# Optimization experiments

Hardware: AMD Instinct MI355X
Metric: run time of the kernel (lower is better)

The kernel has to match this reference:

```python
import jax, jax.numpy as jnp
import numpy as np

V, D, DU, H = 50000, 256, 1024, 128
TEMP = 0.01

def time_cosine_emb(t, d_model):
    half = d_model // 2
    div_term = jnp.exp(jnp.arange(half, dtype=jnp.float32) * (-np.log(10000.0) / half))
    scaled = t[..., None] * div_term  # (B, L, half)
    return jnp.concatenate([jnp.sin(scaled), jnp.cos(scaled)], axis=-1)

def setup_inputs() -> dict:
    key = jax.random.key(0)
    ks = jax.random.split(key, 12)
    B, L = 64, 2048
    q_seq = jax.random.randint(ks[0], (B, L), 0, V)
    r_seq = jax.random.randint(ks[1], (B, L), 0, 3)
    t_seq = jax.random.uniform(ks[2], (B, L), dtype=jnp.float32) * 1000.0
    mask = jnp.ones((B, L), dtype=jnp.float32)
    q_tab = jax.random.normal(ks[3], (V, D), dtype=jnp.float32) * 0.02
    q_tab = q_tab.at[0].set(0.0)  # padding_idx=0
    r_tab = jax.random.normal(ks[4], (3, D), dtype=jnp.float32) * 0.02
    r_tab = r_tab.at[0].set(0.0)  # padding_idx=0
    virtual_node = jax.random.normal(ks[5], (1, D), dtype=jnp.float32)
    Ws1 = jax.random.normal(ks[6], (H, 2 * D), dtype=jnp.float32) * (1.0 / np.sqrt(2 * D))
    bs1 = jnp.zeros((H,), dtype=jnp.float32)
    Ws2 = jax.random.normal(ks[7], (1, H), dtype=jnp.float32) * (1.0 / np.sqrt(H))
    bs2 = jnp.zeros((1,), dtype=jnp.float32)
    Wa = jax.random.normal(ks[8], (DU, D), dtype=jnp.float32) * (1.0 / np.sqrt(D))
    ba = jnp.zeros((DU,), dtype=jnp.float32)
    return {"q_seq": q_seq, "r_seq": r_seq, "t_seq": t_seq, "mask": mask,
            "q_tab": q_tab, "r_tab": r_tab, "virtual_node": virtual_node,
            "Ws1": Ws1, "bs1": bs1, "Ws2": Ws2, "bs2": bs2, "Wa": Wa, "ba": ba}

def reference(q_seq, r_seq, t_seq, mask, q_tab, r_tab, virtual_node, Ws1, bs1, Ws2, bs2, Wa, ba):
    B, L = q_seq.shape
    d_model = q_tab.shape[1]
    # embedding gathers + trig time embedding
    h_events = q_tab[q_seq] + r_tab[r_seq] + time_cosine_emb(t_seq, d_model)  # (B,L,D)
    h_virtual = jnp.broadcast_to(virtual_node[None, :, :], (B, L, d_model))
    pair = jnp.concatenate([h_events, h_virtual], axis=-1)  # (B,L,2D)
    # struct_head: Linear -> LeakyReLU(0.2) -> Linear
    hdn = jax.nn.leaky_relu(jnp.einsum('bld,hd->blh', pair, Ws1) + bs1, 0.2)
    logits = jnp.einsum('blh,oh->blo', hdn, Ws2) + bs2  # (B,L,1)
    A_hat = jax.nn.sigmoid(logits / TEMP) * mask[..., None]
    # aggregator: Linear -> LeakyReLU(0.2)
    h_trans = jax.nn.leaky_relu(jnp.einsum('bld,ud->blu', h_events, Wa) + ba, 0.2)  # (B,L,DU)
    u_i = jnp.sum(h_trans * A_hat, axis=1)  # (B,DU)
    return (u_i, jnp.squeeze(A_hat, -1))
```

## Files before the change

### kernel.cpp

```cpp
#include <hip/hip_runtime.h>

typedef unsigned short ushort_t;
typedef unsigned int uint_t;

typedef short bf16x8 __attribute__((ext_vector_type(8)));
typedef float f32x4 __attribute__((ext_vector_type(4)));

#define MFMA16(a, b, c) __builtin_amdgcn_mfma_f32_16x16x32_bf16(a, b, c, 0, 0, 0)

__device__ __forceinline__ ushort_t f2bf(float f) {
    uint_t u = __float_as_uint(f);
    u += 0x7fffu + ((u >> 16) & 1u);
    return (ushort_t)(u >> 16);
}
__device__ __forceinline__ float bf2f(ushort_t h) {
    return __uint_as_float(((uint_t)h) << 16);
}

__global__ void k_prep(const float* __restrict__ Ws1, const float* __restrict__ bs1,
                       const float* __restrict__ virt, const float* __restrict__ Wa,
                       float* __restrict__ consth, ushort_t* __restrict__ wa_b,
                       ushort_t* __restrict__ ws1h, ushort_t* __restrict__ ws1l) {
    int b = blockIdx.x;
    if (b == 0) {
        int h = threadIdx.x;
        if (h < 128) {
            const float* row = Ws1 + h * 512 + 256;
            float s = bs1[h];
            for (int d = 0; d < 256; ++d) s += row[d] * virt[d];
            consth[h] = s;
        }
        return;
    }
    const float* src;
    int src_stride, tid;
    ushort_t *dhi, *dlo;
    if (b <= 128) {
        tid = (b - 1) * 256 + threadIdx.x;
        src = Wa; src_stride = 256; dhi = wa_b; dlo = nullptr;
    } else {
        tid = (b - 129) * 256 + threadIdx.x;
        src = Ws1; src_stride = 512; dhi = ws1h; dlo = ws1l;
    }
    int pl = tid & 15, kc = (tid >> 4) & 31, pt = tid >> 9;
    int row = pt * 16 + pl;
    const float* s = src + (size_t)row * src_stride + kc * 8;
    ushort_t hs[8], ls[8];
#pragma unroll
    for (int j = 0; j < 8; ++j) {
        float v = s[j];
        ushort_t h = f2bf(v);
        hs[j] = h;
        ls[j] = f2bf(v - bf2f(h));
    }
    uint4 hv;
    hv.x = hs[0] | ((uint_t)hs[1] << 16); hv.y = hs[2] | ((uint_t)hs[3] << 16);
    hv.z = hs[4] | ((uint_t)hs[5] << 16); hv.w = hs[6] | ((uint_t)hs[7] << 16);
    *(uint4*)(dhi + (size_t)tid * 8) = hv;
    if (dlo) {
        uint4 lv;
        lv.x = ls[0] | ((uint_t)ls[1] << 16); lv.y = ls[2] | ((uint_t)ls[3] << 16);
        lv.z = ls[4] | ((uint_t)ls[5] << 16); lv.w = ls[6] | ((uint_t)ls[7] << 16);
        *(uint4*)(dlo + (size_t)tid * 8) = lv;
    }
}

__global__ __launch_bounds__(256, 2) void k_fused(
    const int* __restrict__ q_seq, const int* __restrict__ r_seq,
    const float* __restrict__ t_seq, const float* __restrict__ q_tab,
    const float* __restrict__ r_tab,
    const ushort_t* __restrict__ ws1h, const ushort_t* __restrict__ ws1l,
    const float* __restrict__ consth, const float* __restrict__ Ws2,
    const float* __restrict__ bs2, const float* __restrict__ mask,
    const ushort_t* __restrict__ wa_b, const float* __restrict__ ba,
    float* __restrict__ out_ahat, float* __restrict__ u_i) {
    __shared__ __align__(16) ushort_t sAhi[16384];
    __shared__ __align__(16) ushort_t sAlo[16384];
    __shared__ float sdiv[128];
    __shared__ float sLogit[64];
    __shared__ float sAh[64];
    int tid = threadIdx.x;
    if (tid < 128) sdiv[tid] = __expf((float)tid * -0.07195578415606394f);
    if (tid < 64) sLogit[tid] = 0.0f;
    int w = tid >> 6, lane = tid & 63;
    int pl = lane & 15, kq = lane >> 4;
    int nl = pl;
    int p0 = blockIdx.x * 64;
    int p = p0 + w * 16 + pl;
    int qv = q_seq[p];
    int rr = r_seq[p];
    float tt = t_seq[p];
    const float* grow = q_tab + (size_t)qv * 256;
    const float* rrow = r_tab + (size_t)rr * 256;
    __syncthreads();
#pragma unroll
    for (int it = 0; it < 8; ++it) {
        int kc = it * 4 + kq;
        int k0 = kc * 8;
        float4 qa = *(const float4*)(grow + kc * 8);
        float4 qb = *(const float4*)(grow + kc * 8 + 4);
        float4 ra = *(const float4*)(rrow + kc * 8);
        float4 rb = *(const float4*)(rrow + kc * 8 + 4);
        float v[8] = {qa.x + ra.x, qa.y + ra.y, qa.z + ra.z, qa.w + ra.w,
                      qb.x + rb.x, qb.y + rb.y, qb.z + rb.z, qb.w + rb.w};
        bool iscos = (kc >= 16);
#pragma unroll
        for (int j = 0; j < 8; ++j) {
            float ang = tt * sdiv[(k0 + j) & 127];
            v[j] += iscos ? __cosf(ang) : __sinf(ang);
        }
        ushort_t hs[8], ls[8];
#pragma unroll
        for (int j = 0; j < 8; ++j) {
            ushort_t h = f2bf(v[j]);
            hs[j] = h;
            ls[j] = (ushort_t)(__float_as_uint(v[j] - bf2f(h)) >> 16);
        }
        uint4 hv, lv;
        hv.x = hs[0] | ((uint_t)hs[1] << 16); hv.y = hs[2] | ((uint_t)hs[3] << 16);
        hv.z = hs[4] | ((uint_t)hs[5] << 16); hv.w = hs[6] | ((uint_t)hs[7] << 16);
        lv.x = ls[0] | ((uint_t)ls[1] << 16); lv.y = ls[2] | ((uint_t)ls[3] << 16);
        lv.z = ls[4] | ((uint_t)ls[5] << 16); lv.w = ls[6] | ((uint_t)ls[7] << 16);
        int loff = ((w * 32 + kc) * 16 + pl) * 8;
        *(uint4*)(sAhi + loff) = hv;
        *(uint4*)(sAlo + loff) = lv;
    }
    __syncthreads();
    {
        f32x4 acc[4][2];
        f32x4 z4 = {0.f, 0.f, 0.f, 0.f};
#pragma unroll
        for (int mt = 0; mt < 4; ++mt)
#pragma unroll
            for (int nt = 0; nt < 2; ++nt) acc[mt][nt] = z4;
        bf16x8 bh[2][2], bl[2][2];
#pragma unroll
        for (int nt = 0; nt < 2; ++nt) {
            int off = (((w * 2 + nt) * 32 + kq) * 16 + nl) * 8;
            bh[0][nt] = *(const bf16x8*)(ws1h + off);
            bl[0][nt] = *(const bf16x8*)(ws1l + off);
        }
#pragma unroll
        for (int ks = 0; ks < 8; ++ks) {
            int cur = ks & 1, nxt = cur ^ 1;
            if (ks < 7) {
#pragma unroll
                for (int nt = 0; nt < 2; ++nt) {
                    int off = (((w * 2 + nt) * 32 + (ks + 1) * 4 + kq) * 16 + nl) * 8;
                    bh[nxt][nt] = *(const bf16x8*)(ws1h + off);
                    bl[nxt][nt] = *(const bf16x8*)(ws1l + off);
                }
            }
            bf16x8 ahi[4], alo[4];
#pragma unroll
            for (int mt = 0; mt < 4; ++mt) {
                int off = ((mt * 32 + ks * 4 + kq) * 16 + nl) * 8;
                ahi[mt] = *(const bf16x8*)&sAhi[off];
                alo[mt] = *(const bf16x8*)&sAlo[off];
            }
#pragma unroll
            for (int mt = 0; mt < 4; ++mt)
#pragma unroll
                for (int nt = 0; nt < 2; ++nt) {
                    acc[mt][nt] = MFMA16(ahi[mt], bh[cur][nt], acc[mt][nt]);
                    acc[mt][nt] = MFMA16(alo[mt], bh[cur][nt], acc[mt][nt]);
                    acc[mt][nt] = MFMA16(ahi[mt], bl[cur][nt], acc[mt][nt]);
                }
        }
        float ps[4][4];
#pragma unroll
        for (int mt = 0; mt < 4; ++mt)
#pragma unroll
            for (int r = 0; r < 4; ++r) ps[mt][r] = 0.f;
#pragma unroll
        for (int nt = 0; nt < 2; ++nt) {
            int ng = w * 32 + nt * 16 + nl;
            float chv = consth[ng], w2 = Ws2[ng];
#pragma unroll
            for (int mt = 0; mt < 4; ++mt)
#pragma unroll
                for (int r = 0; r < 4; ++r) {
                    float v = acc[mt][nt][r] + chv;
                    v = v > 0.f ? v : 0.2f * v;
                    ps[mt][r] += v * w2;
                }
        }
#pragma unroll
        for (int mt = 0; mt < 4; ++mt)
#pragma unroll
            for (int r = 0; r < 4; ++r) {
                float x = ps[mt][r];
                x += __shfl_xor(x, 1, 64);
                x += __shfl_xor(x, 2, 64);
                x += __shfl_xor(x, 4, 64);
                x += __shfl_xor(x, 8, 64);
                ps[mt][r] = x;
            }
        if (nl == 0) {
#pragma unroll
            for (int mt = 0; mt < 4; ++mt)
#pragma unroll
                for (int r = 0; r < 4; ++r)
                    atomicAdd(&sLogit[mt * 16 + kq * 4 + r], ps[mt][r]);
        }
    }
    __syncthreads();
    if (tid < 64) {
        int pp = p0 + tid;
        float lg = sLogit[tid] + bs2[0];
        float y = lg * 100.0f;
        y = fminf(fmaxf(y, -60.f), 60.f);
        float a = 1.0f / (1.0f + expf(-y));
        float av = a * mask[pp];
        out_ahat[pp] = av;
        sAh[tid] = av;
    }
    __syncthreads();
    {
        bf16x8 afr[4][8];
#pragma unroll
        for (int mt = 0; mt < 4; ++mt)
#pragma unroll
            for (int ks = 0; ks < 8; ++ks)
                afr[mt][ks] = *(const bf16x8*)&sAhi[((mt * 32 + ks * 4 + kq) * 16 + nl) * 8];
        int bidx = p0 >> 11;
#pragma unroll 1
        for (int nblk = 0; nblk < 4; ++nblk) {
            const ushort_t* gB = wa_b + (size_t)(w * 16 + nblk * 4) * 4096 + lane * 8;
            f32x4 acc[4][4];
            bf16x8 bfr[2][4];
#pragma unroll
            for (int nt = 0; nt < 4; ++nt)
                bfr[0][nt] = *(const bf16x8*)(gB + nt * 4096);
#pragma unroll
            for (int ks = 0; ks < 8; ++ks) {
                int cur = ks & 1, nxt = cur ^ 1;
                if (ks < 7) {
#pragma unroll
                    for (int nt = 0; nt < 4; ++nt)
                        bfr[nxt][nt] = *(const bf16x8*)(gB + nt * 4096 + (ks + 1) * 512);
                }
                if (ks == 0) {
                    f32x4 z4 = {0.f, 0.f, 0.f, 0.f};
#pragma unroll
                    for (int mt = 0; mt < 4; ++mt)
#pragma unroll
                        for (int nt = 0; nt < 4; ++nt)
                            acc[mt][nt] = MFMA16(afr[mt][0], bfr[0][nt], z4);
                } else {
#pragma unroll
                    for (int mt = 0; mt < 4; ++mt)
#pragma unroll
                        for (int nt = 0; nt < 4; ++nt)
                            acc[mt][nt] = MFMA16(afr[mt][ks], bfr[cur][nt], acc[mt][nt]);
                }
            }
#pragma unroll
            for (int nt = 0; nt < 4; ++nt) {
                int ng = w * 256 + nblk * 64 + nt * 16 + nl;
                float ban = ba[ng];
                float s = 0.f;
#pragma unroll
                for (int mt = 0; mt < 4; ++mt)
#pragma unroll
                    for (int r = 0; r < 4; ++r) {
                        float v = acc[mt][nt][r] + ban;
                        v = v > 0.f ? v : 0.2f * v;
                        int ml = mt * 16 + kq * 4 + r;
                        s += v * sAh[ml];
                    }
                s += __shfl_xor(s, 16, 64);
                s += __shfl_xor(s, 32, 64);
                if (kq == 0) atomicAdd(&u_i[bidx * 1024 + ng], s);
            }
        }
    }
}

extern "C" void kernel_launch(void* const* d_in, const int* in_sizes, int n_in,
                              void* d_out, int out_size, void* d_ws, size_t ws_size,
                              hipStream_t stream) {
    const int* q_seq = (const int*)d_in[0];
    const int* r_seq = (const int*)d_in[1];
    const float* t_seq = (const float*)d_in[2];
    const float* mask = (const float*)d_in[3];
    const float* q_tab = (const float*)d_in[4];
    const float* r_tab = (const float*)d_in[5];
    const float* virt = (const float*)d_in[6];
    const float* Ws1 = (const float*)d_in[7];
    const float* bs1 = (const float*)d_in[8];
    const float* Ws2 = (const float*)d_in[9];
    const float* bs2 = (const float*)d_in[10];
    const float* Wa = (const float*)d_in[11];
    const float* ba = (const float*)d_in[12];
    float* out = (float*)d_out;

    ushort_t* wa_b = (ushort_t*)d_ws;
    ushort_t* ws1h = wa_b + 262144;
    ushort_t* ws1l = ws1h + 32768;
    float* ch = (float*)(ws1l + 32768);

    hipMemsetAsync(out, 0, 65536 * sizeof(float), stream);
    hipLaunchKernelGGL(k_prep, dim3(145), dim3(256), 0, stream,
                       Ws1, bs1, virt, Wa, ch, wa_b, ws1h, ws1l);
    hipLaunchKernelGGL(k_fused, dim3(2048), dim3(256), 0, stream,
                       q_seq, r_seq, t_seq, q_tab, r_tab, ws1h, ws1l, ch, Ws2, bs2,
                       mask, wa_b, ba, out + 65536, out);
}
```

Measured before the change: 251.9 us.

## Halve lo-part LDS buffer and drop register-held A fragments to raise occupancy

Shrinks the low-bf16 shared buffer to half size by writing the second half of the K-dimension lo parts from registers mid-loop, behind extra barriers. Stops caching all 32 A fragments in registers for the aggregator GEMM and reloads them from LDS at each k-step, caching the A_hat weights in registers instead. Raises launch bounds to 3 blocks per CU and splits the prep dot-product across 256 threads. The aim is higher occupancy via lower LDS and register use, at the cost of more LDS reads and extra synchronisation.

```diff
diff --git a/kernel.cpp b/kernel.cpp
--- a/kernel.cpp
+++ b/kernel.cpp
@@ -23,13 +23,17 @@
                        ushort_t* __restrict__ ws1h, ushort_t* __restrict__ ws1l) {
     int b = blockIdx.x;
     if (b == 0) {
-        int h = threadIdx.x;
-        if (h < 128) {
-            const float* row = Ws1 + h * 512 + 256;
-            float s = bs1[h];
-            for (int d = 0; d < 256; ++d) s += row[d] * virt[d];
-            consth[h] = s;
-        }
+        __shared__ float sred[256];
+        int t = threadIdx.x;
+        int h = t & 127, half = t >> 7;
+        const float* row = Ws1 + h * 512 + 256 + half * 128;
+        const float* vv = virt + half * 128;
+        float s = 0.f;
+#pragma unroll 4
+        for (int d = 0; d < 128; ++d) s += row[d] * vv[d];
+        sred[t] = s;
+        __syncthreads();
+        if (t < 128) consth[t] = bs1[t] + sred[t] + sred[t + 128];
         return;
     }
     const float* src;
@@ -65,7 +69,7 @@
     }
 }
 
-__global__ __launch_bounds__(256, 2) void k_fused(
+__global__ __launch_bounds__(256, 3) void k_fused(
     const int* __restrict__ q_seq, const int* __restrict__ r_seq,
     const float* __restrict__ t_seq, const float* __restrict__ q_tab,
     const float* __restrict__ r_tab,
@@ -75,7 +79,7 @@
     const ushort_t* __restrict__ wa_b, const float* __restrict__ ba,
     float* __restrict__ out_ahat, float* __restrict__ u_i) {
     __shared__ __align__(16) ushort_t sAhi[16384];
-    __shared__ __align__(16) ushort_t sAlo[16384];
+    __shared__ __align__(16) ushort_t sAlo[8192];
     __shared__ float sdiv[128];
     __shared__ float sLogit[64];
     __shared__ float sAh[64];
@@ -93,6 +97,7 @@
     const float* grow = q_tab + (size_t)qv * 256;
     const float* rrow = r_tab + (size_t)rr * 256;
     __syncthreads();
+    uint4 lo_hold[4];
 #pragma unroll
     for (int it = 0; it < 8; ++it) {
         int kc = it * 4 + kq;
@@ -121,9 +126,12 @@
         hv.z = hs[4] | ((uint_t)hs[5] << 16); hv.w = hs[6] | ((uint_t)hs[7] << 16);
         lv.x = ls[0] | ((uint_t)ls[1] << 16); lv.y = ls[2] | ((uint_t)ls[3] << 16);
         lv.z = ls[4] | ((uint_t)ls[5] << 16); lv.w = ls[6] | ((uint_t)ls[7] << 16);
-        int loff = ((w * 32 + kc) * 16 + pl) * 8;
-        *(uint4*)(sAhi + loff) = hv;
-        *(uint4*)(sAlo + loff) = lv;
+        *(uint4*)(sAhi + ((w * 32 + kc) * 16 + pl) * 8) = hv;
+        if (it < 4) {
+            *(uint4*)(sAlo + ((w * 16 + kc) * 16 + pl) * 8) = lv;
+        } else {
+            lo_hold[it - 4] = lv;
+        }
     }
     __syncthreads();
     {
@@ -142,6 +150,15 @@
         }
 #pragma unroll
         for (int ks = 0; ks < 8; ++ks) {
+            if (ks == 4) {
+                __syncthreads();
+#pragma unroll
+                for (int it = 4; it < 8; ++it) {
+                    int kc = it * 4 + kq;
+                    *(uint4*)(sAlo + ((w * 16 + (kc - 16)) * 16 + pl) * 8) = lo_hold[it - 4];
+                }
+                __syncthreads();
+            }
             int cur = ks & 1, nxt = cur ^ 1;
             if (ks < 7) {
 #pragma unroll
@@ -154,9 +171,8 @@
             bf16x8 ahi[4], alo[4];
 #pragma unroll
             for (int mt = 0; mt < 4; ++mt) {
-                int off = ((mt * 32 + ks * 4 + kq) * 16 + nl) * 8;
-                ahi[mt] = *(const bf16x8*)&sAhi[off];
-                alo[mt] = *(const bf16x8*)&sAlo[off];
+                ahi[mt] = *(const bf16x8*)&sAhi[((mt * 32 + ks * 4 + kq) * 16 + nl) * 8];
+                alo[mt] = *(const bf16x8*)&sAlo[((mt * 16 + (ks & 3) * 4 + kq) * 16 + nl) * 8];
             }
 #pragma unroll
             for (int mt = 0; mt < 4; ++mt)
@@ -181,7 +197,7 @@
 #pragma unroll
                 for (int r = 0; r < 4; ++r) {
                     float v = acc[mt][nt][r] + chv;
-                    v = v > 0.f ? v : 0.2f * v;
+                    v = fmaxf(v, 0.2f * v);
                     ps[mt][r] += v * w2;
                 }
         }
@@ -217,12 +233,11 @@
     }
     __syncthreads();
     {
-        bf16x8 afr[4][8];
+        float ah[16];
 #pragma unroll
         for (int mt = 0; mt < 4; ++mt)
 #pragma unroll
-            for (int ks = 0; ks < 8; ++ks)
-                afr[mt][ks] = *(const bf16x8*)&sAhi[((mt * 32 + ks * 4 + kq) * 16 + nl) * 8];
+            for (int r = 0; r < 4; ++r) ah[mt * 4 + r] = sAh[mt * 16 + kq * 4 + r];
         int bidx = p0 >> 11;
 #pragma unroll 1
         for (int nblk = 0; nblk < 4; ++nblk) {
@@ -240,19 +255,23 @@
                     for (int nt = 0; nt < 4; ++nt)
                         bfr[nxt][nt] = *(const bf16x8*)(gB + nt * 4096 + (ks + 1) * 512);
                 }
+                bf16x8 a_[4];
+#pragma unroll
+                for (int mt = 0; mt < 4; ++mt)
+                    a_[mt] = *(const bf16x8*)&sAhi[((mt * 32 + ks * 4 + kq) * 16 + nl) * 8];
                 if (ks == 0) {
                     f32x4 z4 = {0.f, 0.f, 0.f, 0.f};
 #pragma unroll
                     for (int mt = 0; mt < 4; ++mt)
 #pragma unroll
                         for (int nt = 0; nt < 4; ++nt)
-                            acc[mt][nt] = MFMA16(afr[mt][0], bfr[0][nt], z4);
+                            acc[mt][nt] = MFMA16(a_[mt], bfr[0][nt], z4);
                 } else {
 #pragma unroll
                     for (int mt = 0; mt < 4; ++mt)
 #pragma unroll
                         for (int nt = 0; nt < 4; ++nt)
-                            acc[mt][nt] = MFMA16(afr[mt][ks], bfr[cur][nt], acc[mt][nt]);
+                            acc[mt][nt] = MFMA16(a_[mt], bfr[cur][nt], acc[mt][nt]);
                 }
             }
 #pragma unroll
@@ -265,9 +284,8 @@
 #pragma unroll
                     for (int r = 0; r < 4; ++r) {
                         float v = acc[mt][nt][r] + ban;
-                        v = v > 0.f ? v : 0.2f * v;
-                        int ml = mt * 16 + kq * 4 + r;
-                        s += v * sAh[ml];
+                        v = fmaxf(v, 0.2f * v);
+                        s += v * ah[mt * 4 + r];
                     }
                 s += __shfl_xor(s, 16, 64);
                 s += __shfl_xor(s, 32, 64);
```

Result: slower. 360.8 us (+43.2%).
